# Kernel tuning notes

Hardware: AMD Instinct MI355X
Metric: run time of the kernel (lower is better)

The kernel has to match this reference:

```python
import jax, jax.numpy as jnp
import numpy as np

N, C, SD, A, H = 1048576, 8192, 32, 4, 64


def _xavier(key, shape):
    fan_in, fan_out = shape
    lim = np.sqrt(6.0 / (fan_in + fan_out)).astype(np.float32)
    return jax.random.uniform(key, shape, jnp.float32, -lim, lim)


def setup_inputs() -> dict:
    key = jax.random.key(0)
    ks = jax.random.split(key, 10)
    return {
        "cell_state": jax.random.normal(ks[0], (N, SD), jnp.float32),
        "arch_state": jax.random.uniform(ks[1], (N, A), jnp.float32),
        "energy": jax.random.uniform(ks[2], (N,), jnp.float32),
        "phi_local": jax.random.uniform(ks[3], (N,), jnp.float32),
        "W1": _xavier(ks[4], (SD + A, H)),
        "b1": jnp.zeros((H,), jnp.float32),
        "W2": _xavier(ks[5], (H, 1)),
        "b2": jnp.zeros((1,), jnp.float32),
        "Wc1": _xavier(ks[6], (A + 3, H // 2)),
        "bc1": jnp.zeros((H // 2,), jnp.float32),
        "Wc2": _xavier(ks[7], (H // 2, 1)),
        "bc2": jnp.zeros((1,), jnp.float32),
        "segment_ids": jnp.sort(jax.random.randint(ks[8], (N,), 0, C, jnp.int32)),
        "n_clusters": C,
    }


def reference(cell_state, arch_state, energy, phi_local,
              W1, b1, W2, b2, Wc1, bc1, Wc2, bc2,
              segment_ids, n_clusters):
    seg = segment_ids
    nc = n_clusters
    seg_sum = lambda v: jax.ops.segment_sum(v, seg, num_segments=nc)

    # ---- cells -> clusters ----
    x = jnp.concatenate([cell_state, arch_state], axis=-1)          # [N, SD+A]
    h = jax.nn.relu(x @ W1 + b1)                                    # [N, H]
    base = jax.nn.sigmoid(h @ W2 + b2)[:, 0]                        # [N]
    importance = jnp.clip(base * energy * phi_local, 0.01, 1.0)
    w = importance * energy * phi_local                              # cell weight

    counts = seg_sum(jnp.ones_like(w))                               # [C]
    wsum = seg_sum(w)                                                # [C]
    safe_cnt = jnp.maximum(counts, 1.0)
    # normalized weights; uniform fallback when a cluster's weight sum is 0
    norm_w = jnp.where(wsum[seg] > 0,
                       w / jnp.maximum(wsum, 1e-30)[seg],
                       1.0 / safe_cnt[seg])
    aggregate = seg_sum(norm_w[:, None] * arch_state)                # [C, A]

    # unbiased per-dim variance averaged over dims (torch .var(dim=0).mean())
    mean = seg_sum(arch_state) / safe_cnt[:, None]                   # [C, A]
    sqdev = seg_sum((arch_state - mean[seg]) ** 2)                   # [C, A]
    var = jnp.where(counts >= 2.0,
                    sqdev.mean(-1) / jnp.maximum(counts - 1.0, 1.0),
                    0.0)                                             # [C]
    phi_cluster = 1.0 - jnp.minimum(1.0, var * 2.0)
    coherence = 1.0 - var

    # ---- clusters -> organism ----
    feats = jnp.concatenate([aggregate,
                             phi_cluster[:, None],
                             coherence[:, None],
                             jnp.minimum(1.0, counts / 20.0)[:, None]], axis=-1)  # [C, A+3]
    hc = jax.nn.relu(feats @ Wc1 + bc1)
    basec = jax.nn.sigmoid(hc @ Wc2 + bc2)[:, 0]                     # [C]
    impc = jnp.clip(basec * phi_cluster, 0.01, 1.0)
    valid = counts > 0
    wc = jnp.where(valid, impc * counts, 0.0)
    wc_sum = wc.sum()
    nvalid = jnp.maximum(valid.sum().astype(jnp.float32), 1.0)
    norm_wc = jnp.where(wc_sum > 0,
                        wc / jnp.maximum(wc_sum, 1e-30),
                        valid.astype(jnp.float32) / nvalid)
    global_archetype = (norm_wc[:, None] * aggregate).sum(0)         # [A]

    return aggregate, phi_cluster, coherence, global_archetype
```

## Files before the change

### kernel.cpp

```cpp
#include <hip/hip_runtime.h>
#include <hip/hip_bf16.h>

#define NC 8192
#define SDIM 32
#define ADIM 4
#define XDIM 36
#define HDIM 64
#define CPT 2

typedef _Float16 half8 __attribute__((ext_vector_type(8)));
typedef float f32x4 __attribute__((ext_vector_type(4)));

__device__ __forceinline__ float sigmoidf_(float t) {
    return 1.0f / (1.0f + __expf(-t));
}

__global__ __launch_bounds__(256) void bounds_kernel(
    const int* __restrict__ seg, int* __restrict__ startx,
    int* __restrict__ endx, int n)
{
    const int i = blockIdx.x * 256 + threadIdx.x;
    if (i >= n) return;
    const int s = seg[i];
    if (i == 0 || seg[i - 1] != s) startx[s] = i;
    if (i == n - 1 || seg[i + 1] != s) endx[s] = i + 1;
}

__global__ __launch_bounds__(256, 4) void mlp_kernel(
    const float* __restrict__ cell_state,
    const float* __restrict__ arch_state,
    const float* __restrict__ energy,
    const float* __restrict__ phi_local,
    const float* __restrict__ W1,
    const float* __restrict__ b1,
    const float* __restrict__ W2,
    const float* __restrict__ b2,
    float* __restrict__ w_out,
    int n)
{
    const int tid  = threadIdx.x;
    const int lane = tid & 63;
    const int l15  = lane & 15;
    const int lg   = lane >> 4;

    half8 af[4][2];
    #pragma unroll
    for (int nt = 0; nt < 4; ++nt) {
        #pragma unroll
        for (int s = 0; s < 2; ++s) {
            half8 v = {};
            #pragma unroll
            for (int jj = 0; jj < 8; ++jj) {
                const int k = 32 * s + lg * 8 + jj;
                float wv = 0.0f;
                if (k < XDIM)       wv = W1[k * HDIM + 16 * nt + l15];
                else if (k == XDIM) wv = b1[16 * nt + l15];
                v[jj] = (_Float16)wv;
            }
            af[nt][s] = v;
        }
    }
    float w2v[16];
    #pragma unroll
    for (int nt = 0; nt < 4; ++nt)
        #pragma unroll
        for (int q = 0; q < 4; ++q)
            w2v[nt * 4 + q] = W2[16 * nt + lg * 4 + q];
    const float sb2 = b2[0];

    #pragma unroll 1
    for (int ch = 0; ch < CPT; ++ch) {
        const int chunk_base = blockIdx.x * (256 * CPT) + (tid >> 6) * (64 * CPT) + ch * 64;

        float acc = 0.0f;
        #pragma unroll
        for (int t = 0; t < 4; ++t) {
            int crow = chunk_base + 16 * t + l15;
            if (crow >= n) crow = n - 1;

            const float* cp = cell_state + (size_t)crow * SDIM + lg * 8;
            const float4 f0 = *reinterpret_cast<const float4*>(cp);
            const float4 f1 = *reinterpret_cast<const float4*>(cp + 4);
            half8 x0;
            x0[0] = (_Float16)f0.x; x0[1] = (_Float16)f0.y;
            x0[2] = (_Float16)f0.z; x0[3] = (_Float16)f0.w;
            x0[4] = (_Float16)f1.x; x0[5] = (_Float16)f1.y;
            x0[6] = (_Float16)f1.z; x0[7] = (_Float16)f1.w;

            half8 x1 = {};
            if (lg == 0) {
                const float4 a4 = reinterpret_cast<const float4*>(arch_state)[crow];
                x1[0] = (_Float16)a4.x; x1[1] = (_Float16)a4.y;
                x1[2] = (_Float16)a4.z; x1[3] = (_Float16)a4.w;
                x1[4] = (_Float16)1.0f;
            }

            float pq = 0.0f;
            #pragma unroll
            for (int nt = 0; nt < 4; ++nt) {
                f32x4 c = f32x4{0.f, 0.f, 0.f, 0.f};
                c = __builtin_amdgcn_mfma_f32_16x16x32_f16(af[nt][0], x0, c, 0, 0, 0);
                c = __builtin_amdgcn_mfma_f32_16x16x32_f16(af[nt][1], x1, c, 0, 0, 0);
                #pragma unroll
                for (int q = 0; q < 4; ++q)
                    pq = __builtin_fmaf(fmaxf(c[q], 0.0f), w2v[nt * 4 + q], pq);
            }
            pq += __shfl_xor(pq, 16);
            pq += __shfl_xor(pq, 32);
            if (lg == t) acc = pq;
        }
        const float base = sigmoidf_(acc + sb2);

        const int gid = chunk_base + lane;
        if (gid < n) {
            const float ep = energy[gid] * phi_local[gid];
            const float imp = fminf(fmaxf(base * ep, 0.01f), 1.0f);
            w_out[gid] = imp * ep;
        }
    }
}

__global__ __launch_bounds__(256) void cluster_kernel(
    const float* __restrict__ arch_state,
    const float* __restrict__ w_arr,
    const int*   __restrict__ startx,
    const int*   __restrict__ endx,
    const float* __restrict__ Wc1,
    const float* __restrict__ bc1,
    const float* __restrict__ Wc2,
    const float* __restrict__ bc2,
    float* __restrict__ out,
    float* __restrict__ ws2)
{
    const int lane = threadIdx.x & 63;
    const int c = blockIdx.x * 4 + (threadIdx.x >> 6);
    const int s0 = startx[c];
    const int e0 = endx[c];

    float pw = 0.0f;
    float pa0 = 0.f, pa1 = 0.f, pa2 = 0.f, pa3 = 0.f;
    float pw0 = 0.f, pw1 = 0.f, pw2 = 0.f, pw3 = 0.f;
    float pq0 = 0.f, pq1 = 0.f, pq2 = 0.f, pq3 = 0.f;
    const float4* arch4 = reinterpret_cast<const float4*>(arch_state);
    for (int i = s0 + lane; i < e0; i += 64) {
        const float4 a = arch4[i];
        const float wv = w_arr[i];
        pw += wv;
        pa0 += a.x; pa1 += a.y; pa2 += a.z; pa3 += a.w;
        pw0 = __builtin_fmaf(wv, a.x, pw0); pw1 = __builtin_fmaf(wv, a.y, pw1);
        pw2 = __builtin_fmaf(wv, a.z, pw2); pw3 = __builtin_fmaf(wv, a.w, pw3);
        pq0 = __builtin_fmaf(a.x, a.x, pq0); pq1 = __builtin_fmaf(a.y, a.y, pq1);
        pq2 = __builtin_fmaf(a.z, a.z, pq2); pq3 = __builtin_fmaf(a.w, a.w, pq3);
    }
#define RED13(F) F(pw) F(pa0) F(pa1) F(pa2) F(pa3) \
                 F(pw0) F(pw1) F(pw2) F(pw3) F(pq0) F(pq1) F(pq2) F(pq3)
#define BFLY(V) V += __shfl_xor(V, off_);
    #pragma unroll
    for (int off_ = 1; off_ < 64; off_ <<= 1) { RED13(BFLY) }

    const float cnt = (float)(e0 - s0);
    const float safe_cnt = fmaxf(cnt, 1.0f);
    const float wsum = pw;

    float agg[4];
    if (wsum > 0.0f) {
        const float inv = 1.0f / fmaxf(wsum, 1e-30f);
        agg[0] = pw0 * inv; agg[1] = pw1 * inv;
        agg[2] = pw2 * inv; agg[3] = pw3 * inv;
    } else {
        const float inv = 1.0f / safe_cnt;
        agg[0] = pa0 * inv; agg[1] = pa1 * inv;
        agg[2] = pa2 * inv; agg[3] = pa3 * inv;
    }

    const float sA[4]  = { pa0, pa1, pa2, pa3 };
    const float sA2[4] = { pq0, pq1, pq2, pq3 };
    float sq = 0.0f;
    #pragma unroll
    for (int d = 0; d < 4; ++d) {
        const float mean = sA[d] / safe_cnt;
        const float s2 = sA2[d] - 2.0f * mean * sA[d] + cnt * mean * mean;
        sq += fmaxf(s2, 0.0f);
    }
    const float var = (cnt >= 2.0f) ? (sq * 0.25f) / fmaxf(cnt - 1.0f, 1.0f) : 0.0f;
    const float phi_c = 1.0f - fminf(1.0f, var * 2.0f);
    const float coh = 1.0f - var;

    const float feats[7] = { agg[0], agg[1], agg[2], agg[3],
                             phi_c, coh, fminf(1.0f, cnt * 0.05f) };
    float t = bc2[0];
    #pragma unroll
    for (int j = 0; j < 32; ++j) {
        float hj = bc1[j];
        #pragma unroll
        for (int k = 0; k < 7; ++k)
            hj = __builtin_fmaf(feats[k], Wc1[k * 32 + j], hj);
        t += fmaxf(hj, 0.0f) * Wc2[j];
    }
    const float basec = sigmoidf_(t);
    const float impc = fminf(fmaxf(basec * phi_c, 0.01f), 1.0f);
    const bool valid = cnt > 0.0f;
    const float wc = valid ? impc * cnt : 0.0f;
    const float vf = valid ? 1.0f : 0.0f;

    if (lane == 0) {
        out[c * 4 + 0] = agg[0]; out[c * 4 + 1] = agg[1];
        out[c * 4 + 2] = agg[2]; out[c * 4 + 3] = agg[3];
        out[NC * 4 + c] = phi_c;
        out[NC * 5 + c] = coh;
        ws2[0 * NC + c] = wc;
        ws2[1 * NC + c] = vf;
        #pragma unroll
        for (int d = 0; d < 4; ++d) ws2[(2 + d) * NC + c] = wc * agg[d];
        #pragma unroll
        for (int d = 0; d < 4; ++d) ws2[(6 + d) * NC + c] = vf * agg[d];
    }
}

__global__ __launch_bounds__(1024) void finalize_kernel(
    const float* __restrict__ ws2, float* __restrict__ out)
{
    __shared__ float red[16][10];
    const int tid = threadIdx.x;
    const int lane = tid & 63;
    const int wv = tid >> 6;

    float r[10];
    #pragma unroll
    for (int k = 0; k < 10; ++k) r[k] = 0.0f;
    for (int c = tid; c < NC; c += 1024) {
        #pragma unroll
        for (int k = 0; k < 10; ++k) r[k] += ws2[k * NC + c];
    }
    #pragma unroll
    for (int off = 1; off < 64; off <<= 1) {
        #pragma unroll
        for (int k = 0; k < 10; ++k) r[k] += __shfl_xor(r[k], off);
    }
    if (lane == 0) {
        #pragma unroll
        for (int k = 0; k < 10; ++k) red[wv][k] = r[k];
    }
    __syncthreads();
    if (tid == 0) {
        float g[10];
        #pragma unroll
        for (int k = 0; k < 10; ++k) {
            float acc = 0.0f;
            for (int i = 0; i < 16; ++i) acc += red[i][k];
            g[k] = acc;
        }
        const float wcs = g[0];
        const float nv = fmaxf(g[1], 1.0f);
        #pragma unroll
        for (int d = 0; d < 4; ++d) {
            out[NC * 6 + d] = (wcs > 0.0f) ? g[2 + d] / fmaxf(wcs, 1e-30f)
                                           : g[6 + d] / nv;
        }
    }
}

extern "C" void kernel_launch(void* const* d_in, const int* in_sizes, int n_in,
                              void* d_out, int out_size, void* d_ws, size_t ws_size,
                              hipStream_t stream) {
    const float* cell_state = (const float*)d_in[0];
    const float* arch_state = (const float*)d_in[1];
    const float* energy     = (const float*)d_in[2];
    const float* phi_local  = (const float*)d_in[3];
    const float* W1  = (const float*)d_in[4];
    const float* b1  = (const float*)d_in[5];
    const float* W2  = (const float*)d_in[6];
    const float* b2  = (const float*)d_in[7];
    const float* Wc1 = (const float*)d_in[8];
    const float* bc1 = (const float*)d_in[9];
    const float* Wc2 = (const float*)d_in[10];
    const float* bc2 = (const float*)d_in[11];
    const int* seg   = (const int*)d_in[12];

    const int n = in_sizes[2];
    float* out = (float*)d_out;

    float* w_arr = (float*)d_ws;
    int* startx  = (int*)(w_arr + n);
    int* endx    = startx + NC;
    float* ws2   = (float*)(endx + NC);

    (void)hipMemsetAsync(startx, 0, 2 * NC * sizeof(int), stream);

    bounds_kernel<<<(n + 255) / 256, 256, 0, stream>>>(seg, startx, endx, n);

    const int cells_per_block = 256 * CPT;
    const int nb = (n + cells_per_block - 1) / cells_per_block;
    mlp_kernel<<<nb, 256, 0, stream>>>(cell_state, arch_state, energy, phi_local,
                                       W1, b1, W2, b2, w_arr, n);
    cluster_kernel<<<NC / 4, 256, 0, stream>>>(arch_state, w_arr, startx, endx,
                                               Wc1, bc1, Wc2, bc2, out, ws2);
    finalize_kernel<<<1, 1024, 0, stream>>>(ws2, out);
}
```

Measured before the change: 75.53 us.

## Fuse segment-bounds pass into MLP kernel, prepack W1 fragments, prefetch loads

Removes the separate bounds kernel and folds the segment start/end detection into the MLP kernel through a grid-stride loop. W1 and b1 are converted to half8 MFMA fragments once by a tiny pack kernel, so MLP threads load them directly instead of recomputing them with scattered loads. The MLP kernel now handles one 64-cell chunk per wave with every load issued up front, and the cluster loop software-prefetches the next iteration. The aim is to cut launch count, per-block setup cost and load latency, at the price of a new pack launch and twice as many MLP blocks.

```diff
diff --git a/kernel.cpp b/kernel.cpp
--- a/kernel.cpp
+++ b/kernel.cpp
@@ -6,7 +6,6 @@
 #define ADIM 4
 #define XDIM 36
 #define HDIM 64
-#define CPT 2
 
 typedef _Float16 half8 __attribute__((ext_vector_type(8)));
 typedef float f32x4 __attribute__((ext_vector_type(4)));
@@ -15,35 +14,13 @@
     return 1.0f / (1.0f + __expf(-t));
 }
 
-__global__ __launch_bounds__(256) void bounds_kernel(
-    const int* __restrict__ seg, int* __restrict__ startx,
-    int* __restrict__ endx, int n)
+__global__ void pack_kernel(const float* __restrict__ W1,
+                            const float* __restrict__ b1,
+                            half8* __restrict__ wpack)
 {
-    const int i = blockIdx.x * 256 + threadIdx.x;
-    if (i >= n) return;
-    const int s = seg[i];
-    if (i == 0 || seg[i - 1] != s) startx[s] = i;
-    if (i == n - 1 || seg[i + 1] != s) endx[s] = i + 1;
-}
-
-__global__ __launch_bounds__(256, 4) void mlp_kernel(
-    const float* __restrict__ cell_state,
-    const float* __restrict__ arch_state,
-    const float* __restrict__ energy,
-    const float* __restrict__ phi_local,
-    const float* __restrict__ W1,
-    const float* __restrict__ b1,
-    const float* __restrict__ W2,
-    const float* __restrict__ b2,
-    float* __restrict__ w_out,
-    int n)
-{
-    const int tid  = threadIdx.x;
-    const int lane = tid & 63;
-    const int l15  = lane & 15;
-    const int lg   = lane >> 4;
-
-    half8 af[4][2];
+    const int lane = threadIdx.x;
+    const int l15 = lane & 15;
+    const int lg  = lane >> 4;
     #pragma unroll
     for (int nt = 0; nt < 4; ++nt) {
         #pragma unroll
@@ -57,9 +34,44 @@
                 else if (k == XDIM) wv = b1[16 * nt + l15];
                 v[jj] = (_Float16)wv;
             }
-            af[nt][s] = v;
-        }
-    }
+            wpack[(nt * 2 + s) * 64 + lane] = v;
+        }
+    }
+}
+
+__global__ __launch_bounds__(256, 4) void mlp_kernel(
+    const float* __restrict__ cell_state,
+    const float* __restrict__ arch_state,
+    const float* __restrict__ energy,
+    const float* __restrict__ phi_local,
+    const half8* __restrict__ wpack,
+    const float* __restrict__ W2,
+    const float* __restrict__ b2,
+    const int*   __restrict__ seg,
+    int* __restrict__ startx,
+    int* __restrict__ endx,
+    float* __restrict__ w_out,
+    int n)
+{
+    const int tid  = threadIdx.x;
+    const int lane = tid & 63;
+    const int l15  = lane & 15;
+    const int lg   = lane >> 4;
+    const int gsz  = gridDim.x * 256;
+
+    for (int i = blockIdx.x * 256 + tid; i < n; i += gsz) {
+        const int s = seg[i];
+        if (i == 0 || seg[i - 1] != s) startx[s] = i;
+        if (i == n - 1 || seg[i + 1] != s) endx[s] = i + 1;
+    }
+
+    half8 af[4][2];
+    #pragma unroll
+    for (int nt = 0; nt < 4; ++nt)
+        #pragma unroll
+        for (int s = 0; s < 2; ++s)
+            af[nt][s] = wpack[(nt * 2 + s) * 64 + lane];
+
     float w2v[16];
     #pragma unroll
     for (int nt = 0; nt < 4; ++nt)
@@ -68,55 +80,67 @@
             w2v[nt * 4 + q] = W2[16 * nt + lg * 4 + q];
     const float sb2 = b2[0];
 
-    #pragma unroll 1
-    for (int ch = 0; ch < CPT; ++ch) {
-        const int chunk_base = blockIdx.x * (256 * CPT) + (tid >> 6) * (64 * CPT) + ch * 64;
-
-        float acc = 0.0f;
+    const int chunk_base = blockIdx.x * 256 + (tid >> 6) * 64;
+
+    float4 f0[4], f1[4];
+    #pragma unroll
+    for (int t = 0; t < 4; ++t) {
+        int crow = chunk_base + 16 * t + l15;
+        if (crow >= n) crow = n - 1;
+        const float* cp = cell_state + (size_t)crow * SDIM + lg * 8;
+        f0[t] = *reinterpret_cast<const float4*>(cp);
+        f1[t] = *reinterpret_cast<const float4*>(cp + 4);
+    }
+    float4 a4[4];
+    if (lg == 0) {
         #pragma unroll
         for (int t = 0; t < 4; ++t) {
             int crow = chunk_base + 16 * t + l15;
             if (crow >= n) crow = n - 1;
-
-            const float* cp = cell_state + (size_t)crow * SDIM + lg * 8;
-            const float4 f0 = *reinterpret_cast<const float4*>(cp);
-            const float4 f1 = *reinterpret_cast<const float4*>(cp + 4);
-            half8 x0;
-            x0[0] = (_Float16)f0.x; x0[1] = (_Float16)f0.y;
-            x0[2] = (_Float16)f0.z; x0[3] = (_Float16)f0.w;
-            x0[4] = (_Float16)f1.x; x0[5] = (_Float16)f1.y;
-            x0[6] = (_Float16)f1.z; x0[7] = (_Float16)f1.w;
-
-            half8 x1 = {};
-            if (lg == 0) {
-                const float4 a4 = reinterpret_cast<const float4*>(arch_state)[crow];
-                x1[0] = (_Float16)a4.x; x1[1] = (_Float16)a4.y;
-                x1[2] = (_Float16)a4.z; x1[3] = (_Float16)a4.w;
-                x1[4] = (_Float16)1.0f;
-            }
-
-            float pq = 0.0f;
+            a4[t] = reinterpret_cast<const float4*>(arch_state)[crow];
+        }
+    }
+    const int gid = chunk_base + lane;
+    const int lid = (gid < n) ? gid : (n - 1);
+    const float e = energy[lid];
+    const float p = phi_local[lid];
+
+    float acc = 0.0f;
+    #pragma unroll
+    for (int t = 0; t < 4; ++t) {
+        half8 x0;
+        x0[0] = (_Float16)f0[t].x; x0[1] = (_Float16)f0[t].y;
+        x0[2] = (_Float16)f0[t].z; x0[3] = (_Float16)f0[t].w;
+        x0[4] = (_Float16)f1[t].x; x0[5] = (_Float16)f1[t].y;
+        x0[6] = (_Float16)f1[t].z; x0[7] = (_Float16)f1[t].w;
+
+        half8 x1 = {};
+        if (lg == 0) {
+            x1[0] = (_Float16)a4[t].x; x1[1] = (_Float16)a4[t].y;
+            x1[2] = (_Float16)a4[t].z; x1[3] = (_Float16)a4[t].w;
+            x1[4] = (_Float16)1.0f;
+        }
+
+        float pq = 0.0f;
+        #pragma unroll
+        for (int nt = 0; nt < 4; ++nt) {
+            f32x4 c = f32x4{0.f, 0.f, 0.f, 0.f};
+            c = __builtin_amdgcn_mfma_f32_16x16x32_f16(af[nt][0], x0, c, 0, 0, 0);
+            c = __builtin_amdgcn_mfma_f32_16x16x32_f16(af[nt][1], x1, c, 0, 0, 0);
             #pragma unroll
-            for (int nt = 0; nt < 4; ++nt) {
-                f32x4 c = f32x4{0.f, 0.f, 0.f, 0.f};
-                c = __builtin_amdgcn_mfma_f32_16x16x32_f16(af[nt][0], x0, c, 0, 0, 0);
-                c = __builtin_amdgcn_mfma_f32_16x16x32_f16(af[nt][1], x1, c, 0, 0, 0);
-                #pragma unroll
-                for (int q = 0; q < 4; ++q)
-                    pq = __builtin_fmaf(fmaxf(c[q], 0.0f), w2v[nt * 4 + q], pq);
-            }
-            pq += __shfl_xor(pq, 16);
-            pq += __shfl_xor(pq, 32);
-            if (lg == t) acc = pq;
-        }
-        const float base = sigmoidf_(acc + sb2);
-
-        const int gid = chunk_base + lane;
-        if (gid < n) {
-            const float ep = energy[gid] * phi_local[gid];
-            const float imp = fminf(fmaxf(base * ep, 0.01f), 1.0f);
-            w_out[gid] = imp * ep;
-        }
+            for (int q = 0; q < 4; ++q)
+                pq = __builtin_fmaf(fmaxf(c[q], 0.0f), w2v[nt * 4 + q], pq);
+        }
+        pq += __shfl_xor(pq, 16);
+        pq += __shfl_xor(pq, 32);
+        if (lg == t) acc = pq;
+    }
+    const float base = sigmoidf_(acc + sb2);
+
+    if (gid < n) {
+        const float ep = e * p;
+        const float imp = fminf(fmaxf(base * ep, 0.01f), 1.0f);
+        w_out[gid] = imp * ep;
     }
 }
 
@@ -142,15 +166,23 @@
     float pw0 = 0.f, pw1 = 0.f, pw2 = 0.f, pw3 = 0.f;
     float pq0 = 0.f, pq1 = 0.f, pq2 = 0.f, pq3 = 0.f;
     const float4* arch4 = reinterpret_cast<const float4*>(arch_state);
-    for (int i = s0 + lane; i < e0; i += 64) {
-        const float4 a = arch4[i];
-        const float wv = w_arr[i];
-        pw += wv;
-        pa0 += a.x; pa1 += a.y; pa2 += a.z; pa3 += a.w;
-        pw0 = __builtin_fmaf(wv, a.x, pw0); pw1 = __builtin_fmaf(wv, a.y, pw1);
-        pw2 = __builtin_fmaf(wv, a.z, pw2); pw3 = __builtin_fmaf(wv, a.w, pw3);
-        pq0 = __builtin_fmaf(a.x, a.x, pq0); pq1 = __builtin_fmaf(a.y, a.y, pq1);
-        pq2 = __builtin_fmaf(a.z, a.z, pq2); pq3 = __builtin_fmaf(a.w, a.w, pq3);
+
+    int i = s0 + lane;
+    bool vcur = i < e0;
+    float4 ac = {}; float wcur = 0.0f;
+    if (vcur) { ac = arch4[i]; wcur = w_arr[i]; }
+    while (vcur) {
+        const int j = i + 64;
+        const bool vnext = j < e0;
+        float4 an = {}; float wnext = 0.0f;
+        if (vnext) { an = arch4[j]; wnext = w_arr[j]; }
+        pw += wcur;
+        pa0 += ac.x; pa1 += ac.y; pa2 += ac.z; pa3 += ac.w;
+        pw0 = __builtin_fmaf(wcur, ac.x, pw0); pw1 = __builtin_fmaf(wcur, ac.y, pw1);
+        pw2 = __builtin_fmaf(wcur, ac.z, pw2); pw3 = __builtin_fmaf(wcur, ac.w, pw3);
+        pq0 = __builtin_fmaf(ac.x, ac.x, pq0); pq1 = __builtin_fmaf(ac.y, ac.y, pq1);
+        pq2 = __builtin_fmaf(ac.z, ac.z, pq2); pq3 = __builtin_fmaf(ac.w, ac.w, pq3);
+        i = j; vcur = vnext; ac = an; wcur = wnext;
     }
 #define RED13(F) F(pw) F(pa0) F(pa1) F(pa2) F(pa3) \
                  F(pw0) F(pw1) F(pw2) F(pw3) F(pq0) F(pq1) F(pq2) F(pq3)
@@ -284,15 +316,15 @@
     int* startx  = (int*)(w_arr + n);
     int* endx    = startx + NC;
     float* ws2   = (float*)(endx + NC);
+    half8* wpack = (half8*)(ws2 + 10 * NC);
 
     (void)hipMemsetAsync(startx, 0, 2 * NC * sizeof(int), stream);
 
-    bounds_kernel<<<(n + 255) / 256, 256, 0, stream>>>(seg, startx, endx, n);
-
-    const int cells_per_block = 256 * CPT;
-    const int nb = (n + cells_per_block - 1) / cells_per_block;
+    pack_kernel<<<1, 64, 0, stream>>>(W1, b1, wpack);
+
+    const int nb = (n + 255) / 256;
     mlp_kernel<<<nb, 256, 0, stream>>>(cell_state, arch_state, energy, phi_local,
-                                       W1, b1, W2, b2, w_arr, n);
+                                       wpack, W2, b2, seg, startx, endx, w_arr, n);
     cluster_kernel<<<NC / 4, 256, 0, stream>>>(arch_state, w_arr, startx, endx,
                                                Wc1, bc1, Wc2, bc2, out, ws2);
     finalize_kernel<<<1, 1024, 0, stream>>>(ws2, out);
```

Result: no change. 76.81 us (+1.7%).
